# Optimization experiments

Hardware: AMD Instinct MI355X
Metric: run time of the kernel (lower is better)

Reference implementation:

```python
import jax, jax.numpy as jnp
import numpy as np

# SLAYER SRM-alpha neuron params
THETA = 10.0      # spike threshold
TAU_SR = 10.0     # synaptic (psp) time constant
TAU_REF = 1.0     # refractory time constant
SCALE_REF = 2.0   # refractory scale
TS = 1.0          # simulation step
T_SAMPLE = 156    # simulation window (== tSample)
REF_LEN = 16      # refractory kernel truncation (alpha(tauRef=1) < 1e-4 beyond t=15)

_t = np.arange(T_SAMPLE, dtype=np.float32)
# SRM alpha kernel: eps(t) = t/tau * exp(1 - t/tau)
SRM_KERNEL = jnp.asarray(_t / TAU_SR * np.exp(1.0 - _t / TAU_SR), dtype=jnp.float32)
_tr = np.arange(REF_LEN, dtype=np.float32)
# refractory kernel: -scaleRef*theta * alpha(tauRef)
REF_KERNEL = jnp.asarray(-SCALE_REF * THETA * _tr / TAU_REF * np.exp(1.0 - _tr / TAU_REF), dtype=jnp.float32)

_top_down = [11, 25, 35, 4, 18, 30, 7, 2, 20, 37, 29, 12, 9, 33, 23, 16, 1, 6, 15, 21, 27, 34, 39, 24, 17, 10, 31, 38, 28, 14, 3, 22, 32, 8, 19, 36, 5, 13, 26]
_perm = []
for i in range(39):
    _perm.append(2 * _top_down[i] - 2)
    _perm.append(2 * _top_down[i] - 1)
for i in range(39):
    _perm.append(2 * _top_down[i] - 2 + 78)
    _perm.append(2 * _top_down[i] - 1 + 78)
PERM = jnp.asarray(np.array(_perm, dtype=np.int32))


def dense(x, w):
    # SLAYER dense: linear over channel dim of [N, C, H, W, T]
    return jnp.einsum('nchwt,oc->nohwt', x, w)


def psp(x):
    # causal temporal convolution with the SRM alpha kernel along last axis
    T = x.shape[-1]
    K = SRM_KERNEL.shape[0]
    xf = x.reshape(-1, 1, T)                          # (N*, 1, T)
    k = SRM_KERNEL[::-1].reshape(1, 1, K)             # flip -> causal conv
    y = jax.lax.conv_general_dilated(xf, k, (1,), [(K - 1, 0)])
    return y.reshape(x.shape)


def spike(u):
    # threshold with refractory subtraction: sequential scan over time.
    # pending[d] holds refractory contribution scheduled for time t+d.
    uT = jnp.moveaxis(u, -1, 0)                       # [T, ...]
    R = REF_KERNEL.shape[0]
    ref_next = jnp.concatenate([REF_KERNEL[1:], jnp.zeros((1,), u.dtype)])
    pend0 = jnp.zeros(uT.shape[1:] + (R,), u.dtype)

    def step(pend, u_t):
        u_mod = u_t + pend[..., 0]
        s = (u_mod >= THETA).astype(u.dtype) / TS
        pend = jnp.concatenate([pend[..., 1:], jnp.zeros_like(pend[..., :1])], axis=-1) + s[..., None] * ref_next
        return pend, s

    _, sT = jax.lax.scan(step, pend0, uT)
    return jnp.moveaxis(sT, 0, -1)


def setup_inputs() -> dict:
    key = jax.random.key(0)
    k1, k2, k3, k4, k5 = jax.random.split(key, 5)
    N, C, T, H, OUT = 128, 156, T_SAMPLE, 1024, 20
    x = (jax.random.uniform(k1, (N, C, 1, 1, T)) < 0.1).astype(jnp.float32)
    w_fc1 = jax.random.normal(k2, (H, C), dtype=jnp.float32)
    w_fc2 = jax.random.normal(k3, (OUT, H), dtype=jnp.float32) * 0.1
    w_loc1 = jax.random.normal(k4, (H, T), dtype=jnp.float32)
    w_loc2 = jax.random.normal(k5, (OUT, H), dtype=jnp.float32) * 0.1
    return {"spike_input": x, "w_fc1": w_fc1, "w_fc2": w_fc2, "w_loc1": w_loc1, "w_loc2": w_loc2}


def reference(spike_input, w_fc1, w_fc2, w_loc1, w_loc2):
    # main path
    spike_1 = spike(psp(dense(spike_input, w_fc1)))
    spike_output = spike(psp(dense(spike_1, w_fc2)))
    # location path: swap channel/time dims, permute taxel axis (now last)
    xt = jnp.transpose(spike_input, (0, 4, 2, 3, 1))[..., PERM]
    loc_1 = spike(psp(dense(xt, w_loc1)))
    loc_out = spike(psp(dense(loc_1, w_loc2)))
    return jnp.concatenate([spike_output, loc_out], axis=4)
```

## Files before the change

kernel.cpp:

```cpp
#include <hip/hip_runtime.h>
#include <stdint.h>

#define N_BATCH 128
#define C_IN    156
#define T_SMP   156
#define H_HID   1024
#define O_OUT   20

__constant__ int PERM_C[156] = {
  20,21,48,49,68,69,6,7,34,35,58,59,12,13,2,3,38,39,72,73,56,57,22,23,16,17,
  64,65,44,45,30,31,0,1,10,11,28,29,40,41,52,53,66,67,76,77,46,47,32,33,18,19,
  60,61,74,75,54,55,26,27,4,5,42,43,62,63,14,15,36,37,70,71,8,9,24,25,50,51,
  98,99,126,127,146,147,84,85,112,113,136,137,90,91,80,81,116,117,150,151,134,135,
  100,101,94,95,142,143,122,123,108,109,78,79,88,89,106,107,118,119,130,131,144,145,
  154,155,124,125,110,111,96,97,138,139,152,153,132,133,104,105,82,83,120,121,
  140,141,92,93,114,115,148,149,86,87,102,103,128,129
};

__device__ __constant__ float REFN_C[15] = {
  -20.0f,
  -14.7151776468576930f,
  -8.1201169941967630f,
  -3.9829654694291155f,
  -1.8315638888734178f,
  -0.80855363989025606f,
  -0.34702530473329017f,
  -0.14590111448872258f,
  -0.060383273022452135f,
  -0.024681960817335913f,
  -0.0099879845477466679f,
  -0.0040084081896589585f,
  -0.0015974952118653345f,
  -0.00063348115597555236f,
  -0.00024945861573107036f
};

#define IIR_A  0.904837418035959573
#define IIR_CK 0.271828182845904524

__global__ void __launch_bounds__(256) k_build_lists(
    const float* __restrict__ x,
    uint32_t* __restrict__ lists_m, uint32_t* __restrict__ cnt_m,
    uint32_t* __restrict__ lists_l, uint32_t* __restrict__ cnt_l)
{
  extern __shared__ float xl[];
  const int n = blockIdx.x;
  const float* xn = x + n * (C_IN * T_SMP);
  for (int i = threadIdx.x; i < C_IN * T_SMP; i += 256) xl[i] = xn[i];
  __syncthreads();
  const int t = threadIdx.x;
  if (t < T_SMP) {
    {
      uint32_t* Lp = lists_m + (n * T_SMP + t) * 40;
      uint32_t w = 0; int cnt = 0, nw = 0;
      for (int c = 0; c < C_IN; ++c) {
        if (xl[c * T_SMP + t] > 0.5f) {
          w |= ((uint32_t)c) << ((cnt & 3) * 8);
          ++cnt;
          if ((cnt & 3) == 0) { Lp[nw++] = w; w = 0; }
        }
      }
      if (cnt & 3) {
        for (int k = cnt & 3; k < 4; ++k) w |= 156u << (k * 8);
        Lp[nw++] = w;
      }
      cnt_m[n * T_SMP + t] = (uint32_t)nw;
    }
    {
      uint32_t* Lp = lists_l + (n * T_SMP + t) * 40;
      const int pc = PERM_C[t];
      uint32_t w = 0; int cnt = 0, nw = 0;
      for (int tau = 0; tau < T_SMP; ++tau) {
        if (xl[pc * T_SMP + tau] > 0.5f) {
          w |= ((uint32_t)tau) << ((cnt & 3) * 8);
          ++cnt;
          if ((cnt & 3) == 0) { Lp[nw++] = w; w = 0; }
        }
      }
      if (cnt & 3) {
        for (int k = cnt & 3; k < 4; ++k) w |= 156u << (k * 8);
        Lp[nw++] = w;
      }
      cnt_l[n * T_SMP + t] = (uint32_t)nw;
    }
  }
}

__global__ void __launch_bounds__(256, 2) k_layer1(
    const float* __restrict__ w_fc1, const float* __restrict__ w_loc1,
    const uint32_t* __restrict__ lists_m, const uint32_t* __restrict__ cnt_m,
    const uint32_t* __restrict__ lists_l, const uint32_t* __restrict__ cnt_l,
    uint64_t* __restrict__ s1m_m, uint64_t* __restrict__ s1m_l)
{
  extern __shared__ float wT[];
  const int hc   = blockIdx.x;
  const int n0   = blockIdx.y * 4;
  const int path = blockIdx.z;
  const int tid  = threadIdx.x;
  const float* w = (path == 0) ? w_fc1 : w_loc1;
  const uint32_t* lists = (path == 0) ? lists_m : lists_l;
  const uint32_t* cnts  = (path == 0) ? cnt_m  : cnt_l;
  uint64_t* s1m = (path == 0) ? s1m_m : s1m_l;
  const int h0 = hc * 128;

  {
    const int hp   = tid & 127;
    const int c0   = (tid >> 7) * 78;
    const int slot = 2 * (hp & 63) + (hp >> 6);
    const float* wr = w + (size_t)(h0 + hp) * C_IN + c0;
    #pragma unroll
    for (int k = 0; k < 78; k += 2) {
      float2 v = *(const float2*)(wr + k);
      wT[(c0 + k) * 128 + slot]     = v.x;
      wT[(c0 + k + 1) * 128 + slot] = v.y;
    }
    if (tid < 128) wT[156 * 128 + tid] = 0.0f;
  }
  __syncthreads();

  const int wv   = tid >> 6;
  const int lane = tid & 63;
  const int n    = n0 + wv;
  const int rbase = n * T_SMP;
  const int lx2 = lane * 2;

  float pend[2][15];
  #pragma unroll
  for (int j = 0; j < 2; ++j)
    #pragma unroll
    for (int d = 0; d < 15; ++d) pend[j][d] = 0.0f;
  double e1[2] = {0,0}, e2[2] = {0,0};

  int nw = (int)cnts[rbase];
  uint4 pkA = *(const uint4*)(lists + (size_t)rbase * 40);
  uint4 pkB = *(const uint4*)(lists + (size_t)rbase * 40 + 4);

  for (int t = 0; t < T_SMP; ++t) {
    const int base = rbase + t;
    const int basen = (t < T_SMP - 1) ? base + 1 : base;
    const int nw_n = (int)cnts[basen];
    const uint4 pkA_n = *(const uint4*)(lists + (size_t)basen * 40);
    const uint4 pkB_n = *(const uint4*)(lists + (size_t)basen * 40 + 4);

    double a0[2] = {0,0}, a1[2] = {0,0};

#define DOWORD(PK) do {                                                      \
    uint32_t pk_ = (PK);                                                     \
    int c0_ = pk_ & 255, c1_ = (pk_ >> 8) & 255,                             \
        c2_ = (pk_ >> 16) & 255, c3_ = pk_ >> 24;                            \
    float2 F0 = *(const float2*)&wT[c0_ * 128 + lx2];                        \
    float2 F1 = *(const float2*)&wT[c1_ * 128 + lx2];                        \
    float2 F2 = *(const float2*)&wT[c2_ * 128 + lx2];                        \
    float2 F3 = *(const float2*)&wT[c3_ * 128 + lx2];                        \
    a0[0] += (double)F0.x + (double)F2.x;                                    \
    a1[0] += (double)F1.x + (double)F3.x;                                    \
    a0[1] += (double)F0.y + (double)F2.y;                                    \
    a1[1] += (double)F1.y + (double)F3.y;                                    \
  } while (0)

    if (nw > 0) DOWORD(pkA.x);
    if (nw > 1) DOWORD(pkA.y);
    if (nw > 2) DOWORD(pkA.z);
    if (nw > 3) DOWORD(pkA.w);
    if (nw > 4) DOWORD(pkB.x);
    if (nw > 5) DOWORD(pkB.y);
    if (nw > 6) DOWORD(pkB.z);
    if (nw > 7) DOWORD(pkB.w);
    if (nw > 8) {
      const uint32_t* Lp = lists + (size_t)base * 40;
      for (int wi = 8; wi < nw; ++wi) DOWORD(Lp[wi]);
    }
#undef DOWORD

    uint64_t bal[2];
    #pragma unroll
    for (int j = 0; j < 2; ++j) {
      double upre = a0[j] + a1[j];
      e1[j] = IIR_A * e1[j] + upre;
      e2[j] = IIR_A * e2[j] + e1[j];
      float uf = (float)(IIR_CK * (e2[j] - e1[j]));
      float um = uf + pend[j][0];
      bool sp = (um >= 10.0f);
      float s = sp ? 1.0f : 0.0f;
      #pragma unroll
      for (int d = 0; d < 14; ++d) pend[j][d] = fmaf(s, REFN_C[d], pend[j][d + 1]);
      pend[j][14] = s * REFN_C[14];
      bal[j] = __ballot(sp);
    }
    if (lane == 0) {
      uint64_t* sp_ = s1m + (size_t)base * 16 + hc * 2;
      sp_[0] = bal[0]; sp_[1] = bal[1];
    }
    nw = nw_n; pkA = pkA_n; pkB = pkB_n;
  }
}

__global__ void __launch_bounds__(512, 1) k_layer2(
    const float* __restrict__ w_fc2, const float* __restrict__ w_loc2,
    const uint64_t* __restrict__ s1m_m, const uint64_t* __restrict__ s1m_l,
    float* __restrict__ u2_m, float* __restrict__ u2_l)
{
  extern __shared__ float w2T[];
  const int path = blockIdx.y;
  const int n = blockIdx.x;
  const float* w2 = (path == 0) ? w_fc2 : w_loc2;
  const uint64_t* s1m = (path == 0) ? s1m_m : s1m_l;
  float* u2 = (path == 0) ? u2_m : u2_l;
  for (int i = threadIdx.x; i < O_OUT * H_HID; i += 512) {
    int o = i / H_HID, h = i % H_HID;
    w2T[h * O_OUT + o] = w2[i];
  }
  __syncthreads();
  const int wv   = threadIdx.x >> 6;
  const int lane = threadIdx.x & 63;
  const int hw = lane >> 2, og = lane & 3;

  for (int t = wv; t < T_SMP; t += 8) {
    const int id = n * T_SMP + t;
    uint64_t m = s1m[(size_t)id * 16 + hw];
    double acc0 = 0, acc1 = 0, acc2 = 0, acc3 = 0, acc4 = 0;
    while (m) {
      int b = __builtin_ctzll(m);
      m &= m - 1;
      const float* wp = &w2T[(hw * 64 + b) * O_OUT + og];
      acc0 += (double)wp[0];
      acc1 += (double)wp[4];
      acc2 += (double)wp[8];
      acc3 += (double)wp[12];
      acc4 += (double)wp[16];
    }
    #pragma unroll
    for (int off = 4; off <= 32; off <<= 1) {
      acc0 += __shfl_xor(acc0, off);
      acc1 += __shfl_xor(acc1, off);
      acc2 += __shfl_xor(acc2, off);
      acc3 += __shfl_xor(acc3, off);
      acc4 += __shfl_xor(acc4, off);
    }
    if (lane < 4) {
      u2[((size_t)n * O_OUT + og +  0) * T_SMP + t] = (float)acc0;
      u2[((size_t)n * O_OUT + og +  4) * T_SMP + t] = (float)acc1;
      u2[((size_t)n * O_OUT + og +  8) * T_SMP + t] = (float)acc2;
      u2[((size_t)n * O_OUT + og + 12) * T_SMP + t] = (float)acc3;
      u2[((size_t)n * O_OUT + og + 16) * T_SMP + t] = (float)acc4;
    }
  }
}

__global__ void __launch_bounds__(256) k_psp_spike_out(
    const float* __restrict__ u2_m, const float* __restrict__ u2_l,
    float* __restrict__ out)
{
  const int rid = blockIdx.x * 256 + threadIdx.x;
  const int p = rid / (N_BATCH * O_OUT);
  const int r = rid % (N_BATCH * O_OUT);
  const float* base = ((p == 0) ? u2_m : u2_l) + (size_t)r * T_SMP;
  float* ob = out + (size_t)r * (2 * T_SMP) + p * T_SMP;
  float pend[15];
  #pragma unroll
  for (int d = 0; d < 15; ++d) pend[d] = 0.0f;
  double e1 = 0.0, e2 = 0.0;
  for (int t = 0; t < T_SMP; ++t) {
    double xv = (double)base[t];
    e1 = IIR_A * e1 + xv;
    e2 = IIR_A * e2 + e1;
    float uf = (float)(IIR_CK * (e2 - e1));
    float um = uf + pend[0];
    float s  = (um >= 10.0f) ? 1.0f : 0.0f;
    #pragma unroll
    for (int d = 0; d < 14; ++d) pend[d] = fmaf(s, REFN_C[d], pend[d + 1]);
    pend[14] = s * REFN_C[14];
    ob[t] = s;
  }
}

extern "C" void kernel_launch(void* const* d_in, const int* in_sizes, int n_in,
                              void* d_out, int out_size, void* d_ws, size_t ws_size,
                              hipStream_t stream) {
  const float* x      = (const float*)d_in[0];
  const float* w_fc1  = (const float*)d_in[1];
  const float* w_fc2  = (const float*)d_in[2];
  const float* w_loc1 = (const float*)d_in[3];
  const float* w_loc2 = (const float*)d_in[4];
  float* out = (float*)d_out;
  char* ws = (char*)d_ws;

  uint32_t* lists_m = (uint32_t*)(ws + 0);
  uint32_t* lists_l = (uint32_t*)(ws + 3194880);
  uint32_t* cnt_m   = (uint32_t*)(ws + 6389760);
  uint32_t* cnt_l   = (uint32_t*)(ws + 6469632);
  uint64_t* s1m_m   = (uint64_t*)(ws + 6549504);
  uint64_t* s1m_l   = (uint64_t*)(ws + 9105408);
  float*    u2_m    = (float*)   (ws + 11661312);
  float*    u2_l    = (float*)   (ws + 13258752);

  hipLaunchKernelGGL(k_build_lists, dim3(128), dim3(256),
                     C_IN * T_SMP * sizeof(float), stream,
                     x, lists_m, cnt_m, lists_l, cnt_l);
  hipLaunchKernelGGL(k_layer1, dim3(8, 32, 2), dim3(256),
                     157 * 128 * sizeof(float), stream,
                     w_fc1, w_loc1, lists_m, cnt_m, lists_l, cnt_l, s1m_m, s1m_l);
  hipLaunchKernelGGL(k_layer2, dim3(128, 2), dim3(512),
                     H_HID * O_OUT * sizeof(float), stream,
                     w_fc2, w_loc2, s1m_m, s1m_l, u2_m, u2_l);
  hipLaunchKernelGGL(k_psp_spike_out, dim3(20), dim3(256), 0, stream,
                     u2_m, u2_l, out);
}
```

Baseline: 354.9 us.

## Halve per-thread hidden units in layer1 and split layer2 over time chunks

Layer1 now assigns one hidden unit per lane (64 per block) instead of two, doubling the grid and raising the launch-bounds occupancy target to 4 blocks per CU, with half the shared weight tile. Packed spike indices are made wave-uniform with readfirstlane. Layer2 splits each sample's 156 timesteps into four blocks of 39 to get more blocks. The aim is more parallelism and shorter serial dependency chains per thread, at the cost of redundant list reads and per-block weight staging.

```diff
diff --git a/kernel.cpp b/kernel.cpp
--- a/kernel.cpp
+++ b/kernel.cpp
@@ -86,7 +86,7 @@
   }
 }
 
-__global__ void __launch_bounds__(256, 2) k_layer1(
+__global__ void __launch_bounds__(256, 4) k_layer1(
     const float* __restrict__ w_fc1, const float* __restrict__ w_loc1,
     const uint32_t* __restrict__ lists_m, const uint32_t* __restrict__ cnt_m,
     const uint32_t* __restrict__ lists_l, const uint32_t* __restrict__ cnt_l,
@@ -101,20 +101,15 @@
   const uint32_t* lists = (path == 0) ? lists_m : lists_l;
   const uint32_t* cnts  = (path == 0) ? cnt_m  : cnt_l;
   uint64_t* s1m = (path == 0) ? s1m_m : s1m_l;
-  const int h0 = hc * 128;
+  const int h0 = hc * 64;
 
   {
-    const int hp   = tid & 127;
-    const int c0   = (tid >> 7) * 78;
-    const int slot = 2 * (hp & 63) + (hp >> 6);
+    const int hp = tid & 63;
+    const int c0 = (tid >> 6) * 39;
     const float* wr = w + (size_t)(h0 + hp) * C_IN + c0;
     #pragma unroll
-    for (int k = 0; k < 78; k += 2) {
-      float2 v = *(const float2*)(wr + k);
-      wT[(c0 + k) * 128 + slot]     = v.x;
-      wT[(c0 + k + 1) * 128 + slot] = v.y;
-    }
-    if (tid < 128) wT[156 * 128 + tid] = 0.0f;
+    for (int k = 0; k < 39; ++k) wT[(c0 + k) * 64 + hp] = wr[k];
+    if (tid < 64) wT[156 * 64 + tid] = 0.0f;
   }
   __syncthreads();
 
@@ -122,14 +117,11 @@
   const int lane = tid & 63;
   const int n    = n0 + wv;
   const int rbase = n * T_SMP;
-  const int lx2 = lane * 2;
-
-  float pend[2][15];
+
+  float pend[15];
   #pragma unroll
-  for (int j = 0; j < 2; ++j)
-    #pragma unroll
-    for (int d = 0; d < 15; ++d) pend[j][d] = 0.0f;
-  double e1[2] = {0,0}, e2[2] = {0,0};
+  for (int d = 0; d < 15; ++d) pend[d] = 0.0f;
+  double e1 = 0.0, e2 = 0.0;
 
   int nw = (int)cnts[rbase];
   uint4 pkA = *(const uint4*)(lists + (size_t)rbase * 40);
@@ -142,20 +134,18 @@
     const uint4 pkA_n = *(const uint4*)(lists + (size_t)basen * 40);
     const uint4 pkB_n = *(const uint4*)(lists + (size_t)basen * 40 + 4);
 
-    double a0[2] = {0,0}, a1[2] = {0,0};
+    double a0 = 0.0, a1 = 0.0;
 
 #define DOWORD(PK) do {                                                      \
-    uint32_t pk_ = (PK);                                                     \
+    uint32_t pk_ = __builtin_amdgcn_readfirstlane(PK);                       \
     int c0_ = pk_ & 255, c1_ = (pk_ >> 8) & 255,                             \
         c2_ = (pk_ >> 16) & 255, c3_ = pk_ >> 24;                            \
-    float2 F0 = *(const float2*)&wT[c0_ * 128 + lx2];                        \
-    float2 F1 = *(const float2*)&wT[c1_ * 128 + lx2];                        \
-    float2 F2 = *(const float2*)&wT[c2_ * 128 + lx2];                        \
-    float2 F3 = *(const float2*)&wT[c3_ * 128 + lx2];                        \
-    a0[0] += (double)F0.x + (double)F2.x;                                    \
-    a1[0] += (double)F1.x + (double)F3.x;                                    \
-    a0[1] += (double)F0.y + (double)F2.y;                                    \
-    a1[1] += (double)F1.y + (double)F3.y;                                    \
+    float F0 = wT[c0_ * 64 + lane];                                          \
+    float F1 = wT[c1_ * 64 + lane];                                          \
+    float F2 = wT[c2_ * 64 + lane];                                          \
+    float F3 = wT[c3_ * 64 + lane];                                          \
+    a0 += (double)F0 + (double)F2;                                           \
+    a1 += (double)F1 + (double)F3;                                           \
   } while (0)
 
     if (nw > 0) DOWORD(pkA.x);
@@ -172,25 +162,19 @@
     }
 #undef DOWORD
 
-    uint64_t bal[2];
-    #pragma unroll
-    for (int j = 0; j < 2; ++j) {
-      double upre = a0[j] + a1[j];
-      e1[j] = IIR_A * e1[j] + upre;
-      e2[j] = IIR_A * e2[j] + e1[j];
-      float uf = (float)(IIR_CK * (e2[j] - e1[j]));
-      float um = uf + pend[j][0];
-      bool sp = (um >= 10.0f);
-      float s = sp ? 1.0f : 0.0f;
-      #pragma unroll
-      for (int d = 0; d < 14; ++d) pend[j][d] = fmaf(s, REFN_C[d], pend[j][d + 1]);
-      pend[j][14] = s * REFN_C[14];
-      bal[j] = __ballot(sp);
-    }
-    if (lane == 0) {
-      uint64_t* sp_ = s1m + (size_t)base * 16 + hc * 2;
-      sp_[0] = bal[0]; sp_[1] = bal[1];
-    }
+    double upre = a0 + a1;
+    e1 = IIR_A * e1 + upre;
+    e2 = IIR_A * e2 + e1;
+    float uf = (float)(IIR_CK * (e2 - e1));
+    float um = uf + pend[0];
+    bool sp = (um >= 10.0f);
+    float s = sp ? 1.0f : 0.0f;
+    #pragma unroll
+    for (int d = 0; d < 14; ++d) pend[d] = fmaf(s, REFN_C[d], pend[d + 1]);
+    pend[14] = s * REFN_C[14];
+    uint64_t bal = __ballot(sp);
+    if (lane == 0) s1m[(size_t)base * 16 + hc] = bal;
+
     nw = nw_n; pkA = pkA_n; pkB = pkB_n;
   }
 }
@@ -202,7 +186,8 @@
 {
   extern __shared__ float w2T[];
   const int path = blockIdx.y;
-  const int n = blockIdx.x;
+  const int n  = blockIdx.x >> 2;
+  const int tc = blockIdx.x & 3;
   const float* w2 = (path == 0) ? w_fc2 : w_loc2;
   const uint64_t* s1m = (path == 0) ? s1m_m : s1m_l;
   float* u2 = (path == 0) ? u2_m : u2_l;
@@ -215,7 +200,8 @@
   const int lane = threadIdx.x & 63;
   const int hw = lane >> 2, og = lane & 3;
 
-  for (int t = wv; t < T_SMP; t += 8) {
+  for (int tt = wv; tt < 39; tt += 8) {
+    const int t = tc * 39 + tt;
     const int id = n * T_SMP + t;
     uint64_t m = s1m[(size_t)id * 16 + hw];
     double acc0 = 0, acc1 = 0, acc2 = 0, acc3 = 0, acc4 = 0;
@@ -297,10 +283,10 @@
   hipLaunchKernelGGL(k_build_lists, dim3(128), dim3(256),
                      C_IN * T_SMP * sizeof(float), stream,
                      x, lists_m, cnt_m, lists_l, cnt_l);
-  hipLaunchKernelGGL(k_layer1, dim3(8, 32, 2), dim3(256),
-                     157 * 128 * sizeof(float), stream,
+  hipLaunchKernelGGL(k_layer1, dim3(16, 32, 2), dim3(256),
+                     157 * 64 * sizeof(float), stream,
                      w_fc1, w_loc1, lists_m, cnt_m, lists_l, cnt_l, s1m_m, s1m_l);
-  hipLaunchKernelGGL(k_layer2, dim3(128, 2), dim3(512),
+  hipLaunchKernelGGL(k_layer2, dim3(512, 2), dim3(512),
                      H_HID * O_OUT * sizeof(float), stream,
                      w_fc2, w_loc2, s1m_m, s1m_l, u2_m, u2_l);
   hipLaunchKernelGGL(k_psp_spike_out, dim3(20), dim3(256), 0, stream,
```

Measured after the change: 346.8 us. -2.3%, faster.
